# Kernel tuning notes

Hardware: AMD Instinct MI355X
Metric: run time of the kernel (lower is better)

The kernel has to match this reference:

```python
import jax, jax.numpy as jnp
import numpy as np

B, T, E, H = 128, 512, 256, 256  # batch, seqlen, embed_size, latent_size (must be equal E==H)


def gru_cell(x, h, Wih, Whh, bih, bhh):
    # PyTorch GRU gate math. Wih:[3H,E], Whh:[3H,H]
    gi = x @ Wih.T + bih  # [B,3H]
    gh = h @ Whh.T + bhh  # [B,3H]
    i_r, i_z, i_n = jnp.split(gi, 3, axis=-1)
    h_r, h_z, h_n = jnp.split(gh, 3, axis=-1)
    r = jax.nn.sigmoid(i_r + h_r)
    z = jax.nn.sigmoid(i_z + h_z)
    n = jnp.tanh(i_n + r * h_n)
    return (1.0 - z) * n + z * h


def setup_inputs() -> dict:
    key = jax.random.key(0)
    ks = jax.random.split(key, 9)
    s = 1.0 / np.sqrt(H)  # PyTorch default init scale
    return {
        "x": jax.random.normal(ks[0], (B, T, E), dtype=jnp.float32),
        "Wih_e": jax.random.normal(ks[1], (3 * H, E), dtype=jnp.float32) * s,
        "Whh_e": jax.random.normal(ks[2], (3 * H, H), dtype=jnp.float32) * s,
        "bih_e": jax.random.normal(ks[3], (3 * H,), dtype=jnp.float32) * s,
        "bhh_e": jax.random.normal(ks[4], (3 * H,), dtype=jnp.float32) * s,
        "Wih_d": jax.random.normal(ks[5], (3 * H, E), dtype=jnp.float32) * s,
        "Whh_d": jax.random.normal(ks[6], (3 * H, H), dtype=jnp.float32) * s,
        "bih_d": jax.random.normal(ks[7], (3 * H,), dtype=jnp.float32) * s,
        "bhh_d": jax.random.normal(ks[8], (3 * H,), dtype=jnp.float32) * s,
    }


def reference(x, Wih_e, Whh_e, bih_e, bhh_e, Wih_d, Whh_d, bih_d, bhh_d):
    Bs = x.shape[0]
    h0 = jnp.zeros((Bs, H), dtype=x.dtype)

    # ---- encode: nn.GRU, return final hidden state as latents ----
    def enc_step(h, xt):
        return gru_cell(xt, h, Wih_e, Whh_e, bih_e, bhh_e), None

    latents, _ = jax.lax.scan(enc_step, h0, x.transpose(1, 0, 2))  # [B,H]

    # ---- decode: GRUCell unroll; input=prev output, hidden=prev output ----
    def dec_step(carry, _):
        inp, state = carry
        hx = gru_cell(inp, state, Wih_d, Whh_d, bih_d, bhh_d)
        return (hx, hx), hx

    _, ys = jax.lax.scan(dec_step, (latents, h0), None, length=T)  # [T,B,H]
    # original prepends each step's output, so stacked order is reversed
    outputs = jnp.flip(ys, axis=0).transpose(1, 0, 2)  # [B,T,H]
    return outputs, latents
```

## Files before the change

kernel.cpp:

```cpp
#include <hip/hip_runtime.h>


typedef unsigned short u16;
typedef unsigned int   u32;

typedef _Float16 f16x8 __attribute__((ext_vector_type(8)));
typedef float    f32x4 __attribute__((ext_vector_type(4)));

#define B_ 128
#define T_ 512
#define H_ 256
#define G3 768

#define GI_OFF     0ull
#define WIH_OFF    100663296ull
#define WHH_OFF    101056512ull
#define WRZ_OFF    101449728ull
#define WIN_OFF    101711872ull
#define WHN_OFF    101842944ull
#define BG_OFF     101974016ull
#define BHN_E_OFF  101977088ull
#define BDEC_OFF   101978112ull
#define H1_OFF     101982208ull

#define E_WN1_L   0
#define E_STG_L   65536
#define E_HL_L    116736
#define E_BHN_L   133120
#define ENC_LDS   134144

#define D_WHN_L   0
#define D_HL_L    131072
#define D_BIA_L   147456
#define DEC_LDS   151552

__device__ __forceinline__ float h2f(u16 u) {
    return (float)__builtin_bit_cast(_Float16, u);
}
__device__ __forceinline__ u16 f2h(float f) {
    _Float16 h = (_Float16)f;
    return __builtin_bit_cast(u16, h);
}
__device__ __forceinline__ float sigf(float x) {
    return __builtin_amdgcn_rcpf(1.f + __builtin_amdgcn_exp2f(x * -1.4426950408889634f));
}
__device__ __forceinline__ float tanhf_(float x) {
    return 1.f - 2.f * __builtin_amdgcn_rcpf(1.f + __builtin_amdgcn_exp2f(x * 2.8853900817779268f));
}
__device__ __forceinline__ f16x8 ldfrag(const u16* base, int nt, int ks, int l) {
    return __builtin_bit_cast(f16x8, *(const uint4*)(base + ((size_t)((nt * 8 + ks) * 64 + l)) * 8));
}
__device__ __forceinline__ void gload_lds16(const void* g, void* l) {
    __builtin_amdgcn_global_load_lds(
        (const __attribute__((address_space(1))) unsigned int*)(g),
        (__attribute__((address_space(3))) unsigned int*)(l),
        16, 0, 0);
}
#define MFMA16(a, b, c) __builtin_amdgcn_mfma_f32_16x16x32_f16((a), (b), (c), 0, 0, 0)

__global__ __launch_bounds__(256) void prep_kernel(
    const float* __restrict__ Wih_e, const float* __restrict__ Whh_e,
    const float* __restrict__ bih_e, const float* __restrict__ bhh_e,
    const float* __restrict__ Wih_d, const float* __restrict__ Whh_d,
    const float* __restrict__ bih_d, const float* __restrict__ bhh_d,
    char* ws)
{
    int gid = blockIdx.x * 256 + threadIdx.x;
    const int NFRAG = 160 * 8 * 64;
    if (gid < NFRAG) {
        int lane = gid & 63;
        int ks = (gid >> 6) & 7;
        int a = gid >> 9;
        int lm = lane & 15, lg = lane >> 4;
        int k0 = ks * 32 + lg * 8;
        const float* s0; const float* s1 = nullptr; u16* dst; int nt;
        if (a < 48)       { nt = a;       s0 = Wih_e + (size_t)(nt*16+lm)*256 + k0;            dst = (u16*)(ws + WIH_OFF); }
        else if (a < 96)  { nt = a - 48;  s0 = Whh_e + (size_t)(nt*16+lm)*256 + k0;            dst = (u16*)(ws + WHH_OFF); }
        else if (a < 128) { nt = a - 96;  s0 = Wih_d + (size_t)(nt*16+lm)*256 + k0;
                            s1 = Whh_d + (size_t)(nt*16+lm)*256 + k0;                          dst = (u16*)(ws + WRZ_OFF); }
        else if (a < 144) { nt = a - 128; s0 = Wih_d + (size_t)(512+nt*16+lm)*256 + k0;        dst = (u16*)(ws + WIN_OFF); }
        else              { nt = a - 144; s0 = Whh_d + (size_t)(512+nt*16+lm)*256 + k0;        dst = (u16*)(ws + WHN_OFF); }
        u32 wd[4];
        #pragma unroll
        for (int p = 0; p < 4; ++p) {
            float v0 = s0[2*p]   + (s1 ? s1[2*p]   : 0.f);
            float v1 = s0[2*p+1] + (s1 ? s1[2*p+1] : 0.f);
            wd[p] = (u32)f2h(v0) | ((u32)f2h(v1) << 16);
        }
        uint4 o; o.x = wd[0]; o.y = wd[1]; o.z = wd[2]; o.w = wd[3];
        *(uint4*)(dst + ((size_t)((nt * 8 + ks) * 64 + lane)) * 8) = o;
    } else if (gid < NFRAG + 2048) {
        int bid = gid - NFRAG;
        if (bid < 768) {
            ((float*)(ws + BG_OFF))[bid] = bih_e[bid] + (bid < 512 ? bhh_e[bid] : 0.f);
        } else if (bid < 1024) {
            int j = bid - 768;  ((float*)(ws + BHN_E_OFF))[j] = bhh_e[512 + j];
        } else if (bid < 1536) {
            int j = bid - 1024; ((float*)(ws + BDEC_OFF))[j] = bih_d[j] + bhh_d[j];
        } else if (bid < 1792) {
            int j = bid - 1536; ((float*)(ws + BDEC_OFF))[512 + j] = bih_d[512 + j];
        } else {
            int j = bid - 1792; ((float*)(ws + BDEC_OFF))[768 + j] = bhh_d[512 + j];
        }
    }
}

__global__ __launch_bounds__(256) void gemm_gi(const float* __restrict__ x, char* ws)
{
    extern __shared__ char smem[];
    ushort4* xl = (ushort4*)smem;
    const u16* Wfrag = (const u16*)(ws + WIH_OFF);
    const float* bias = (const float*)(ws + BG_OFF);
    u16* gi = (u16*)(ws + GI_OFF);
    int tid = threadIdx.x;
    int m0 = blockIdx.x * 128;
    int n0 = blockIdx.y * 128;
    {
        int row = tid >> 1, half = tid & 1;
        const float* src = x + (size_t)(m0 + row) * 256 + half * 128;
        #pragma unroll
        for (int q = 0; q < 32; ++q) {
            f32x4 v = *(const f32x4*)(src + q * 4);
            int vv = (row << 6) + (half * 32 + q);
            vv ^= ((row & 7) << 1);
            xl[vv] = make_ushort4(f2h(v.x), f2h(v.y), f2h(v.z), f2h(v.w));
        }
    }
    __syncthreads();
    int l = tid & 63, w = tid >> 6;
    int lm = l & 15, lg = l >> 4;
    int gh = w >> 1, mh = w & 1;
    const f32x4 Z4 = {0.f, 0.f, 0.f, 0.f};
    f32x4 acc[4][4];
    #pragma unroll
    for (int a = 0; a < 4; ++a)
        #pragma unroll
        for (int b = 0; b < 4; ++b) acc[a][b] = Z4;
    #pragma unroll
    for (int ks = 0; ks < 8; ++ks) {
        f16x8 xf[4], wf[4];
        #pragma unroll
        for (int mt = 0; mt < 4; ++mt) {
            int row = mh * 64 + mt * 16 + lm;
            int vv = (row << 6) + ((ks * 4 + lg) << 1);
            vv ^= ((row & 7) << 1);
            xf[mt] = __builtin_bit_cast(f16x8, *(const uint4*)&xl[vv]);
        }
        #pragma unroll
        for (int gt = 0; gt < 4; ++gt)
            wf[gt] = ldfrag(Wfrag, (n0 >> 4) + gh * 4 + gt, ks, l);
        #pragma unroll
        for (int gt = 0; gt < 4; ++gt)
            #pragma unroll
            for (int mt = 0; mt < 4; ++mt)
                acc[gt][mt] = MFMA16(wf[gt], xf[mt], acc[gt][mt]);
    }
    #pragma unroll
    for (int gt = 0; gt < 4; ++gt) {
        int g0 = n0 + (gh * 4 + gt) * 16 + lg * 4;
        f32x4 bv = *(const f32x4*)(bias + g0);
        #pragma unroll
        for (int mt = 0; mt < 4; ++mt) {
            int m = m0 + mh * 64 + mt * 16 + lm;
            f32x4 v = acc[gt][mt] + bv;
            *(ushort4*)(gi + (size_t)m * 768 + g0) =
                make_ushort4(f2h(v.x), f2h(v.y), f2h(v.z), f2h(v.w));
        }
    }
}

__global__ __launch_bounds__(512, 2) void enc_kernel(char* ws, float* __restrict__ dout)
{
    extern __shared__ char smem[];
    uint4*   wn1   = (uint4*)(smem + E_WN1_L);
    char*    stg   = smem + E_STG_L;
    ushort4* hl    = (ushort4*)(smem + E_HL_L);
    float*   bhn_l = (float*)(smem + E_BHN_L);
    const u16* Wf = (const u16*)(ws + WHH_OFF);
    const u16* gi = (const u16*)(ws + GI_OFF);
    float* lat = dout + (size_t)B_ * T_ * H_;
    int tid = threadIdx.x;
    int l = tid & 63, w = tid >> 6;
    int lm = l & 15, lg = l >> 4, lg4 = lg * 4;
    int b0 = blockIdx.x * 16;

    if (tid < 256) bhn_l[tid] = ((const float*)(ws + BHN_E_OFF))[tid];
    #pragma unroll
    for (int q = 0; q < 2; ++q) hl[tid + q * 512] = make_ushort4(0, 0, 0, 0);
    #pragma unroll
    for (int p = 0; p < 8; ++p) {
        int u = tid + p * 512;
        int no = u >> 9, ks = (u >> 6) & 7, ll = u & 63;
        wn1[u] = *(const uint4*)(Wf + ((size_t)(((32 + 2 * no + 1) * 8 + ks) * 64 + ll)) * 8);
    }
    f16x8 Wr[2][8], Wz[2][8], Wn0[8];
    #pragma unroll
    for (int i = 0; i < 2; ++i)
        #pragma unroll
        for (int ks = 0; ks < 8; ++ks) {
            Wr[i][ks] = ldfrag(Wf, 2 * w + i, ks, l);
            Wz[i][ks] = ldfrag(Wf, 16 + 2 * w + i, ks, l);
        }
    #pragma unroll
    for (int ks = 0; ks < 8; ++ks) Wn0[ks] = ldfrag(Wf, 32 + 2 * w, ks, l);

    u32 goff[4];
    #pragma unroll
    for (int q = 0; q < 4; ++q) {
        int s = w + q * 8; if (s > 24) s = 24;
        int u = s * 64 + l;
        int row = u / 100, c = u % 100; if (c > 95) c = 95;
        goff[q] = ((u32)(b0 + row) * T_) * G3 + (u32)c * 8;
    }
    {
        #pragma unroll
        for (int q = 0; q < 4; ++q) {
            int s = w + q * 8;
            if (q < 3 || w == 0)
                gload_lds16(gi + goff[q], stg + s * 1024);
        }
    }
    __syncthreads();

    const f32x4 Z4 = {0.f, 0.f, 0.f, 0.f};
    f32x4 hreg[2] = {Z4, Z4};
    int cur = 0;

    for (int t = 0; t < 512; ++t) {
        int nxt = cur ^ 1;
        int tn = (t + 1) & 511;
        {
            char* sb = stg + nxt * 25600;
            #pragma unroll
            for (int q = 0; q < 4; ++q) {
                int s = w + q * 8;
                if (q < 3 || w == 0)
                    gload_lds16(gi + goff[q] + (u32)tn * G3, sb + s * 1024);
            }
        }
        const ushort4* hc = hl + cur * 1024;
        ushort4* hd = hl + nxt * 1024;
        const char* sc = stg + cur * 25600;

        f32x4 aR[2], aZ[2], aN[2];
        #pragma unroll
        for (int i = 0; i < 2; ++i) { aR[i] = Z4; aZ[i] = Z4; aN[i] = Z4; }
        #pragma unroll
        for (int ks = 0; ks < 8; ++ks) {
            int vv = (lm << 6) + ((ks * 4 + lg) << 1);
            vv ^= ((lm & 7) << 1);
            f16x8 hb = __builtin_bit_cast(f16x8, *(const uint4*)&hc[vv]);
            f16x8 wn1v = __builtin_bit_cast(f16x8, wn1[(w * 8 + ks) * 64 + l]);
            aR[0] = MFMA16(Wr[0][ks], hb, aR[0]);
            aZ[0] = MFMA16(Wz[0][ks], hb, aZ[0]);
            aN[0] = MFMA16(Wn0[ks],   hb, aN[0]);
            aR[1] = MFMA16(Wr[1][ks], hb, aR[1]);
            aZ[1] = MFMA16(Wz[1][ks], hb, aZ[1]);
            aN[1] = MFMA16(wn1v,      hb, aN[1]);
        }
        ushort4 hnew[2];
        const char* rb = sc + lm * 1600;
        #pragma unroll
        for (int i = 0; i < 2; ++i) {
            int j0 = (2 * w + i) * 16 + lg4;
            ushort4 gR = *(const ushort4*)(rb + j0 * 2);
            ushort4 gZ = *(const ushort4*)(rb + 512 + j0 * 2);
            ushort4 gN = *(const ushort4*)(rb + 1024 + j0 * 2);
            float bn0 = bhn_l[j0], bn1 = bhn_l[j0 + 1], bn2 = bhn_l[j0 + 2], bn3 = bhn_l[j0 + 3];
            float r0 = sigf(h2f(gR.x) + aR[i].x), z0 = sigf(h2f(gZ.x) + aZ[i].x);
            float n0 = tanhf_(h2f(gN.x) + r0 * (aN[i].x + bn0));
            float h0 = n0 + z0 * (hreg[i].x - n0);
            float r1 = sigf(h2f(gR.y) + aR[i].y), z1 = sigf(h2f(gZ.y) + aZ[i].y);
            float n1 = tanhf_(h2f(gN.y) + r1 * (aN[i].y + bn1));
            float h1 = n1 + z1 * (hreg[i].y - n1);
            float r2 = sigf(h2f(gR.z) + aR[i].z), z2 = sigf(h2f(gZ.z) + aZ[i].z);
            float n2 = tanhf_(h2f(gN.z) + r2 * (aN[i].z + bn2));
            float h2 = n2 + z2 * (hreg[i].z - n2);
            float r3 = sigf(h2f(gR.w) + aR[i].w), z3 = sigf(h2f(gZ.w) + aZ[i].w);
            float n3 = tanhf_(h2f(gN.w) + r3 * (aN[i].w + bn3));
            float h3 = n3 + z3 * (hreg[i].w - n3);
            f32x4 hv = {h0, h1, h2, h3};
            hreg[i] = hv;
            hnew[i] = make_ushort4(f2h(h0), f2h(h1), f2h(h2), f2h(h3));
            if (t == 511) *(f32x4*)(lat + (size_t)(b0 + lm) * 256 + j0) = hv;
        }
        #pragma unroll
        for (int i = 0; i < 2; ++i) {
            int j0 = (2 * w + i) * 16 + lg4;
            int vh = (lm << 6) + (j0 >> 2);
            vh ^= ((lm & 7) << 1);
            hd[vh] = hnew[i];
        }
        __syncthreads();
        cur = nxt;
    }
}

__global__ __launch_bounds__(256) void dec0_kernel(
    const float* __restrict__ Wih_d, const float* __restrict__ bih_d,
    const float* __restrict__ bhh_d, char* ws, float* __restrict__ dout)
{
    __shared__ float latl[256];
    int b = blockIdx.x, j = threadIdx.x;
    const float* latg = dout + (size_t)B_ * T_ * H_;
    latl[j] = latg[(size_t)b * 256 + j];
    __syncthreads();
    const float* wr = Wih_d + (size_t)j * 256;
    const float* wz = Wih_d + (size_t)(256 + j) * 256;
    const float* wn = Wih_d + (size_t)(512 + j) * 256;
    float sr = 0.f, sz = 0.f, sn = 0.f;
    #pragma unroll 4
    for (int k = 0; k < 256; ++k) {
        float h = latl[k];
        sr = fmaf(h, wr[k], sr); sz = fmaf(h, wz[k], sz); sn = fmaf(h, wn[k], sn);
    }
    float r = sigf(sr + bih_d[j] + bhh_d[j]);
    float z = sigf(sz + bih_d[256 + j] + bhh_d[256 + j]);
    float n = tanhf_(sn + bih_d[512 + j] + r * bhh_d[512 + j]);
    float h1v = (1.f - z) * n;
    ((float*)(ws + H1_OFF))[(size_t)b * 256 + j] = h1v;
    dout[((size_t)b * 512 + 511) * 256 + j] = h1v;
}

__global__ __launch_bounds__(512, 2) void dec_kernel(char* ws, float* __restrict__ dout)
{
    extern __shared__ char smem[];
    uint4*   whn    = (uint4*)(smem + D_WHN_L);
    ushort4* hl     = (ushort4*)(smem + D_HL_L);
    float*   bias_l = (float*)(smem + D_BIA_L);
    const u16* Wrzf = (const u16*)(ws + WRZ_OFF);
    const u16* Winf = (const u16*)(ws + WIN_OFF);
    const uint4* Whnf = (const uint4*)(ws + WHN_OFF);
    const float* bdec = (const float*)(ws + BDEC_OFF);
    const float* h1 = (const float*)(ws + H1_OFF);
    int tid = threadIdx.x;
    int l = tid & 63, w = tid >> 6;
    int lm = l & 15, lg = l >> 4, lg4 = lg * 4;
    int b0 = blockIdx.x * 16;

    #pragma unroll
    for (int p = 0; p < 16; ++p) { int u = tid + p * 512; whn[u] = Whnf[u]; }
    #pragma unroll
    for (int q = 0; q < 2; ++q) bias_l[tid + q * 512] = bdec[tid + q * 512];
    #pragma unroll
    for (int q = 0; q < 2; ++q) {
        int u = tid + q * 512;
        int row = u >> 6, cu = u & 63;
        const float* s = h1 + (size_t)(b0 + row) * 256 + cu * 4;
        int vv = u ^ ((row & 7) << 1);
        hl[vv] = make_ushort4(f2h(s[0]), f2h(s[1]), f2h(s[2]), f2h(s[3]));
    }
    f16x8 Wr[2][8], Wz[2][8], Wi[2][8];
    #pragma unroll
    for (int i = 0; i < 2; ++i)
        #pragma unroll
        for (int ks = 0; ks < 8; ++ks) {
            Wr[i][ks] = ldfrag(Wrzf, 2 * w + i, ks, l);
            Wz[i][ks] = ldfrag(Wrzf, 16 + 2 * w + i, ks, l);
            Wi[i][ks] = ldfrag(Winf, 2 * w + i, ks, l);
        }
    const f32x4 Z4 = {0.f, 0.f, 0.f, 0.f};
    f32x4 hreg[2];
    #pragma unroll
    for (int i = 0; i < 2; ++i) {
        int j0 = (2 * w + i) * 16 + lg4;
        hreg[i] = *(const f32x4*)(h1 + (size_t)(b0 + lm) * 256 + j0);
    }
    __syncthreads();
    int cur = 0;

    for (int it = 1; it < 512; ++it) {
        int nxt = cur ^ 1;
        int trow = 511 - it;
        const ushort4* hc = hl + cur * 1024;
        ushort4* hd = hl + nxt * 1024;

        f32x4 aR[2], aZ[2], aI[2], aN[2];
        #pragma unroll
        for (int i = 0; i < 2; ++i) {
            int jb = (2 * w + i) * 16 + lg4;
            aR[i] = *(const f32x4*)(bias_l + jb);
            aZ[i] = *(const f32x4*)(bias_l + 256 + jb);
            aI[i] = *(const f32x4*)(bias_l + 512 + jb);
            aN[i] = Z4;
        }
        #pragma unroll
        for (int ks = 0; ks < 8; ++ks) {
            int vv = (lm << 6) + ((ks * 4 + lg) << 1);
            vv ^= ((lm & 7) << 1);
            f16x8 hb = __builtin_bit_cast(f16x8, *(const uint4*)&hc[vv]);
            f16x8 wn0 = __builtin_bit_cast(f16x8, whn[((2 * w) * 8 + ks) * 64 + l]);
            f16x8 wn1 = __builtin_bit_cast(f16x8, whn[((2 * w + 1) * 8 + ks) * 64 + l]);
            aR[0] = MFMA16(Wr[0][ks], hb, aR[0]);
            aZ[0] = MFMA16(Wz[0][ks], hb, aZ[0]);
            aI[0] = MFMA16(Wi[0][ks], hb, aI[0]);
            aN[0] = MFMA16(wn0,       hb, aN[0]);
            aR[1] = MFMA16(Wr[1][ks], hb, aR[1]);
            aZ[1] = MFMA16(Wz[1][ks], hb, aZ[1]);
            aI[1] = MFMA16(Wi[1][ks], hb, aI[1]);
            aN[1] = MFMA16(wn1,       hb, aN[1]);
        }
        ushort4 hnew[2];
        #pragma unroll
        for (int i = 0; i < 2; ++i) {
            int jb = (2 * w + i) * 16 + lg4;
            float bn0 = bias_l[768 + jb], bn1 = bias_l[768 + jb + 1];
            float bn2 = bias_l[768 + jb + 2], bn3 = bias_l[768 + jb + 3];
            float r0 = sigf(aR[i].x), z0 = sigf(aZ[i].x);
            float n0 = tanhf_(aI[i].x + r0 * (aN[i].x + bn0));
            float h0 = n0 + z0 * (hreg[i].x - n0);
            float r1 = sigf(aR[i].y), z1 = sigf(aZ[i].y);
            float n1 = tanhf_(aI[i].y + r1 * (aN[i].y + bn1));
            float h1v = n1 + z1 * (hreg[i].y - n1);
            float r2 = sigf(aR[i].z), z2 = sigf(aZ[i].z);
            float n2 = tanhf_(aI[i].z + r2 * (aN[i].z + bn2));
            float h2 = n2 + z2 * (hreg[i].z - n2);
            float r3 = sigf(aR[i].w), z3 = sigf(aZ[i].w);
            float n3 = tanhf_(aI[i].w + r3 * (aN[i].w + bn3));
            float h3 = n3 + z3 * (hreg[i].w - n3);
            f32x4 hv = {h0, h1v, h2, h3};
            hreg[i] = hv;
            hnew[i] = make_ushort4(f2h(h0), f2h(h1v), f2h(h2), f2h(h3));
            *(f32x4*)(dout + ((size_t)(b0 + lm) * 512 + trow) * 256 + jb) = hv;
        }
        #pragma unroll
        for (int i = 0; i < 2; ++i) {
            int j0 = (2 * w + i) * 16 + lg4;
            int vh = (lm << 6) + (j0 >> 2);
            vh ^= ((lm & 7) << 1);
            hd[vh] = hnew[i];
        }
        __syncthreads();
        cur = nxt;
    }
}

extern "C" void kernel_launch(void* const* d_in, const int* in_sizes, int n_in,
                              void* d_out, int out_size, void* d_ws, size_t ws_size,
                              hipStream_t stream)
{
    const float* x     = (const float*)d_in[0];
    const float* Wih_e = (const float*)d_in[1];
    const float* Whh_e = (const float*)d_in[2];
    const float* bih_e = (const float*)d_in[3];
    const float* bhh_e = (const float*)d_in[4];
    const float* Wih_d = (const float*)d_in[5];
    const float* Whh_d = (const float*)d_in[6];
    const float* bih_d = (const float*)d_in[7];
    const float* bhh_d = (const float*)d_in[8];
    char* ws = (char*)d_ws;
    float* out = (float*)d_out;

    (void)hipFuncSetAttribute((const void*)gemm_gi, hipFuncAttributeMaxDynamicSharedMemorySize, 65536);
    (void)hipFuncSetAttribute((const void*)enc_kernel, hipFuncAttributeMaxDynamicSharedMemorySize, ENC_LDS);
    (void)hipFuncSetAttribute((const void*)dec_kernel, hipFuncAttributeMaxDynamicSharedMemorySize, DEC_LDS);

    prep_kernel<<<328, 256, 0, stream>>>(Wih_e, Whh_e, bih_e, bhh_e,
                                         Wih_d, Whh_d, bih_d, bhh_d, ws);
    gemm_gi<<<dim3(512, 6), 256, 65536, stream>>>(x, ws);
    enc_kernel<<<8, 512, ENC_LDS, stream>>>(ws, out);
    dec0_kernel<<<128, 256, 0, stream>>>(Wih_d, bih_d, bhh_d, ws, out);
    dec_kernel<<<8, 512, DEC_LDS, stream>>>(ws, out);
}
```

Measured before the change: 2.271 ms.

## Keep all recurrent weight fragments in registers and restructure per-step MFMA chains

```diff
diff --git a/kernel.cpp b/kernel.cpp
--- a/kernel.cpp
+++ b/kernel.cpp
@@ -5,6 +5,7 @@
 typedef unsigned int   u32;
 
 typedef _Float16 f16x8 __attribute__((ext_vector_type(8)));
+typedef _Float16 f16x2 __attribute__((ext_vector_type(2)));
 typedef float    f32x4 __attribute__((ext_vector_type(4)));
 
 #define B_ 128
@@ -23,16 +24,9 @@
 #define BDEC_OFF   101978112ull
 #define H1_OFF     101982208ull
 
-#define E_WN1_L   0
-#define E_STG_L   65536
-#define E_HL_L    116736
-#define E_BHN_L   133120
-#define ENC_LDS   134144
-
-#define D_WHN_L   0
-#define D_HL_L    131072
-#define D_BIA_L   147456
-#define DEC_LDS   151552
+#define E_STG_L   0
+#define E_HL_L    51200
+#define ENC_LDS   67584
 
 __device__ __forceinline__ float h2f(u16 u) {
     return (float)__builtin_bit_cast(_Float16, u);
@@ -40,6 +34,9 @@
 __device__ __forceinline__ u16 f2h(float f) {
     _Float16 h = (_Float16)f;
     return __builtin_bit_cast(u16, h);
+}
+__device__ __forceinline__ u32 pk2(float a, float b) {
+    return __builtin_bit_cast(u32, __builtin_amdgcn_cvt_pkrtz(a, b));
 }
 __device__ __forceinline__ float sigf(float x) {
     return __builtin_amdgcn_rcpf(1.f + __builtin_amdgcn_exp2f(x * -1.4426950408889634f));
@@ -172,10 +169,8 @@
 __global__ __launch_bounds__(512, 2) void enc_kernel(char* ws, float* __restrict__ dout)
 {
     extern __shared__ char smem[];
-    uint4*   wn1   = (uint4*)(smem + E_WN1_L);
-    char*    stg   = smem + E_STG_L;
-    ushort4* hl    = (ushort4*)(smem + E_HL_L);
-    float*   bhn_l = (float*)(smem + E_BHN_L);
+    char*    stg = smem + E_STG_L;
+    ushort4* hl  = (ushort4*)(smem + E_HL_L);
     const u16* Wf = (const u16*)(ws + WHH_OFF);
     const u16* gi = (const u16*)(ws + GI_OFF);
     float* lat = dout + (size_t)B_ * T_ * H_;
@@ -184,25 +179,22 @@
     int lm = l & 15, lg = l >> 4, lg4 = lg * 4;
     int b0 = blockIdx.x * 16;
 
-    if (tid < 256) bhn_l[tid] = ((const float*)(ws + BHN_E_OFF))[tid];
     #pragma unroll
     for (int q = 0; q < 2; ++q) hl[tid + q * 512] = make_ushort4(0, 0, 0, 0);
-    #pragma unroll
-    for (int p = 0; p < 8; ++p) {
-        int u = tid + p * 512;
-        int no = u >> 9, ks = (u >> 6) & 7, ll = u & 63;
-        wn1[u] = *(const uint4*)(Wf + ((size_t)(((32 + 2 * no + 1) * 8 + ks) * 64 + ll)) * 8);
-    }
-    f16x8 Wr[2][8], Wz[2][8], Wn0[8];
+
+    f16x8 Wr[2][8], Wz[2][8], Wn[2][8];
     #pragma unroll
     for (int i = 0; i < 2; ++i)
         #pragma unroll
         for (int ks = 0; ks < 8; ++ks) {
             Wr[i][ks] = ldfrag(Wf, 2 * w + i, ks, l);
             Wz[i][ks] = ldfrag(Wf, 16 + 2 * w + i, ks, l);
-        }
-    #pragma unroll
-    for (int ks = 0; ks < 8; ++ks) Wn0[ks] = ldfrag(Wf, 32 + 2 * w, ks, l);
+            Wn[i][ks] = ldfrag(Wf, 32 + 2 * w + i, ks, l);
+        }
+    f32x4 bnb[2];
+    #pragma unroll
+    for (int i = 0; i < 2; ++i)
+        bnb[i] = *(const f32x4*)((const float*)(ws + BHN_E_OFF) + (2 * w + i) * 16 + lg4);
 
     u32 goff[4];
     #pragma unroll
@@ -240,56 +232,55 @@
         }
         const ushort4* hc = hl + cur * 1024;
         ushort4* hd = hl + nxt * 1024;
-        const char* sc = stg + cur * 25600;
-
-        f32x4 aR[2], aZ[2], aN[2];
-        #pragma unroll
-        for (int i = 0; i < 2; ++i) { aR[i] = Z4; aZ[i] = Z4; aN[i] = Z4; }
+        const char* rb = stg + cur * 25600 + lm * 1600;
+
+        f16x8 hb[8];
         #pragma unroll
         for (int ks = 0; ks < 8; ++ks) {
             int vv = (lm << 6) + ((ks * 4 + lg) << 1);
             vv ^= ((lm & 7) << 1);
-            f16x8 hb = __builtin_bit_cast(f16x8, *(const uint4*)&hc[vv]);
-            f16x8 wn1v = __builtin_bit_cast(f16x8, wn1[(w * 8 + ks) * 64 + l]);
-            aR[0] = MFMA16(Wr[0][ks], hb, aR[0]);
-            aZ[0] = MFMA16(Wz[0][ks], hb, aZ[0]);
-            aN[0] = MFMA16(Wn0[ks],   hb, aN[0]);
-            aR[1] = MFMA16(Wr[1][ks], hb, aR[1]);
-            aZ[1] = MFMA16(Wz[1][ks], hb, aZ[1]);
-            aN[1] = MFMA16(wn1v,      hb, aN[1]);
-        }
-        ushort4 hnew[2];
-        const char* rb = sc + lm * 1600;
+            hb[ks] = __builtin_bit_cast(f16x8, *(const uint4*)&hc[vv]);
+        }
+        ushort4 gR[2], gZ[2], gN[2];
         #pragma unroll
         for (int i = 0; i < 2; ++i) {
             int j0 = (2 * w + i) * 16 + lg4;
-            ushort4 gR = *(const ushort4*)(rb + j0 * 2);
-            ushort4 gZ = *(const ushort4*)(rb + 512 + j0 * 2);
-            ushort4 gN = *(const ushort4*)(rb + 1024 + j0 * 2);
-            float bn0 = bhn_l[j0], bn1 = bhn_l[j0 + 1], bn2 = bhn_l[j0 + 2], bn3 = bhn_l[j0 + 3];
-            float r0 = sigf(h2f(gR.x) + aR[i].x), z0 = sigf(h2f(gZ.x) + aZ[i].x);
-            float n0 = tanhf_(h2f(gN.x) + r0 * (aN[i].x + bn0));
+            gR[i] = *(const ushort4*)(rb + j0 * 2);
+            gZ[i] = *(const ushort4*)(rb + 512 + j0 * 2);
+            gN[i] = *(const ushort4*)(rb + 1024 + j0 * 2);
+        }
+        #pragma unroll
+        for (int i = 0; i < 2; ++i) {
+            int j0 = (2 * w + i) * 16 + lg4;
+            f32x4 aR = {h2f(gR[i].x), h2f(gR[i].y), h2f(gR[i].z), h2f(gR[i].w)};
+            f32x4 aZ = {h2f(gZ[i].x), h2f(gZ[i].y), h2f(gZ[i].z), h2f(gZ[i].w)};
+            f32x4 aN = Z4;
+            __builtin_amdgcn_s_setprio(1);
+            #pragma unroll
+            for (int ks = 0; ks < 8; ++ks) {
+                aR = MFMA16(Wr[i][ks], hb[ks], aR);
+                aZ = MFMA16(Wz[i][ks], hb[ks], aZ);
+                aN = MFMA16(Wn[i][ks], hb[ks], aN);
+            }
+            __builtin_amdgcn_s_setprio(0);
+            float r0 = sigf(aR.x), z0 = sigf(aZ.x);
+            float n0 = tanhf_(h2f(gN[i].x) + r0 * (aN.x + bnb[i].x));
             float h0 = n0 + z0 * (hreg[i].x - n0);
-            float r1 = sigf(h2f(gR.y) + aR[i].y), z1 = sigf(h2f(gZ.y) + aZ[i].y);
-            float n1 = tanhf_(h2f(gN.y) + r1 * (aN[i].y + bn1));
+            float r1 = sigf(aR.y), z1 = sigf(aZ.y);
+            float n1 = tanhf_(h2f(gN[i].y) + r1 * (aN.y + bnb[i].y));
             float h1 = n1 + z1 * (hreg[i].y - n1);
-            float r2 = sigf(h2f(gR.z) + aR[i].z), z2 = sigf(h2f(gZ.z) + aZ[i].z);
-            float n2 = tanhf_(h2f(gN.z) + r2 * (aN[i].z + bn2));
+            float r2 = sigf(aR.z), z2 = sigf(aZ.z);
+            float n2 = tanhf_(h2f(gN[i].z) + r2 * (aN.z + bnb[i].z));
             float h2 = n2 + z2 * (hreg[i].z - n2);
-            float r3 = sigf(h2f(gR.w) + aR[i].w), z3 = sigf(h2f(gZ.w) + aZ[i].w);
-            float n3 = tanhf_(h2f(gN.w) + r3 * (aN[i].w + bn3));
+            float r3 = sigf(aR.w), z3 = sigf(aZ.w);
+            float n3 = tanhf_(h2f(gN[i].w) + r3 * (aN.w + bnb[i].w));
             float h3 = n3 + z3 * (hreg[i].w - n3);
             f32x4 hv = {h0, h1, h2, h3};
             hreg[i] = hv;
-            hnew[i] = make_ushort4(f2h(h0), f2h(h1), f2h(h2), f2h(h3));
-            if (t == 511) *(f32x4*)(lat + (size_t)(b0 + lm) * 256 + j0) = hv;
-        }
-        #pragma unroll
-        for (int i = 0; i < 2; ++i) {
-            int j0 = (2 * w + i) * 16 + lg4;
             int vh = (lm << 6) + (j0 >> 2);
             vh ^= ((lm & 7) << 1);
-            hd[vh] = hnew[i];
+            *(uint2*)&hd[vh] = make_uint2(pk2(h0, h1), pk2(h2, h3));
+            if (t == 511) *(f32x4*)(lat + (size_t)(b0 + lm) * 256 + j0) = hv;
         }
         __syncthreads();
         cur = nxt;
@@ -324,13 +315,10 @@
 
 __global__ __launch_bounds__(512, 2) void dec_kernel(char* ws, float* __restrict__ dout)
 {
-    extern __shared__ char smem[];
-    uint4*   whn    = (uint4*)(smem + D_WHN_L);
-    ushort4* hl     = (ushort4*)(smem + D_HL_L);
-    float*   bias_l = (float*)(smem + D_BIA_L);
+    __shared__ ushort4 hl[2][1024];
     const u16* Wrzf = (const u16*)(ws + WRZ_OFF);
     const u16* Winf = (const u16*)(ws + WIN_OFF);
-    const uint4* Whnf = (const uint4*)(ws + WHN_OFF);
+    const u16* Whnf = (const u16*)(ws + WHN_OFF);
     const float* bdec = (const float*)(ws + BDEC_OFF);
     const float* h1 = (const float*)(ws + H1_OFF);
     int tid = threadIdx.x;
@@ -339,18 +327,14 @@
     int b0 = blockIdx.x * 16;
 
     #pragma unroll
-    for (int p = 0; p < 16; ++p) { int u = tid + p * 512; whn[u] = Whnf[u]; }
-    #pragma unroll
-    for (int q = 0; q < 2; ++q) bias_l[tid + q * 512] = bdec[tid + q * 512];
-    #pragma unroll
     for (int q = 0; q < 2; ++q) {
         int u = tid + q * 512;
         int row = u >> 6, cu = u & 63;
         const float* s = h1 + (size_t)(b0 + row) * 256 + cu * 4;
         int vv = u ^ ((row & 7) << 1);
-        hl[vv] = make_ushort4(f2h(s[0]), f2h(s[1]), f2h(s[2]), f2h(s[3]));
-    }
-    f16x8 Wr[2][8], Wz[2][8], Wi[2][8];
+        hl[0][vv] = make_ushort4(f2h(s[0]), f2h(s[1]), f2h(s[2]), f2h(s[3]));
+    }
+    f16x8 Wr[2][8], Wz[2][8], Wi[2][8], Wn[2][8];
     #pragma unroll
     for (int i = 0; i < 2; ++i)
         #pragma unroll
@@ -358,7 +342,17 @@
             Wr[i][ks] = ldfrag(Wrzf, 2 * w + i, ks, l);
             Wz[i][ks] = ldfrag(Wrzf, 16 + 2 * w + i, ks, l);
             Wi[i][ks] = ldfrag(Winf, 2 * w + i, ks, l);
-        }
+            Wn[i][ks] = ldfrag(Whnf, 2 * w + i, ks, l);
+        }
+    f32x4 bR[2], bZ[2], bI[2], bN[2];
+    #pragma unroll
+    for (int i = 0; i < 2; ++i) {
+        int jb = (2 * w + i) * 16 + lg4;
+        bR[i] = *(const f32x4*)(bdec + jb);
+        bZ[i] = *(const f32x4*)(bdec + 256 + jb);
+        bI[i] = *(const f32x4*)(bdec + 512 + jb);
+        bN[i] = *(const f32x4*)(bdec + 768 + jb);
+    }
     const f32x4 Z4 = {0.f, 0.f, 0.f, 0.f};
     f32x4 hreg[2];
     #pragma unroll
@@ -372,63 +366,47 @@
     for (int it = 1; it < 512; ++it) {
         int nxt = cur ^ 1;
         int trow = 511 - it;
-        const ushort4* hc = hl + cur * 1024;
-        ushort4* hd = hl + nxt * 1024;
-
-        f32x4 aR[2], aZ[2], aI[2], aN[2];
-        #pragma unroll
-        for (int i = 0; i < 2; ++i) {
-            int jb = (2 * w + i) * 16 + lg4;
-            aR[i] = *(const f32x4*)(bias_l + jb);
-            aZ[i] = *(const f32x4*)(bias_l + 256 + jb);
-            aI[i] = *(const f32x4*)(bias_l + 512 + jb);
-            aN[i] = Z4;
-        }
+        const ushort4* hc = hl[cur];
+        ushort4* hd = hl[nxt];
+
+        f16x8 hb[8];
         #pragma unroll
         for (int ks = 0; ks < 8; ++ks) {
             int vv = (lm << 6) + ((ks * 4 + lg) << 1);
             vv ^= ((lm & 7) << 1);
-            f16x8 hb = __builtin_bit_cast(f16x8, *(const uint4*)&hc[vv]);
-            f16x8 wn0 = __builtin_bit_cast(f16x8, whn[((2 * w) * 8 + ks) * 64 + l]);
-            f16x8 wn1 = __builtin_bit_cast(f16x8, whn[((2 * w + 1) * 8 + ks) * 64 + l]);
-            aR[0] = MFMA16(Wr[0][ks], hb, aR[0]);
-            aZ[0] = MFMA16(Wz[0][ks], hb, aZ[0]);
-            aI[0] = MFMA16(Wi[0][ks], hb, aI[0]);
-            aN[0] = MFMA16(wn0,       hb, aN[0]);
-            aR[1] = MFMA16(Wr[1][ks], hb, aR[1]);
-            aZ[1] = MFMA16(Wz[1][ks], hb, aZ[1]);
-            aI[1] = MFMA16(Wi[1][ks], hb, aI[1]);
-            aN[1] = MFMA16(wn1,       hb, aN[1]);
-        }
-        ushort4 hnew[2];
+            hb[ks] = __builtin_bit_cast(f16x8, *(const uint4*)&hc[vv]);
+        }
         #pragma unroll
         for (int i = 0; i < 2; ++i) {
             int jb = (2 * w + i) * 16 + lg4;
-            float bn0 = bias_l[768 + jb], bn1 = bias_l[768 + jb + 1];
-            float bn2 = bias_l[768 + jb + 2], bn3 = bias_l[768 + jb + 3];
-            float r0 = sigf(aR[i].x), z0 = sigf(aZ[i].x);
-            float n0 = tanhf_(aI[i].x + r0 * (aN[i].x + bn0));
+            f32x4 aR = bR[i], aZ = bZ[i], aI = bI[i], aN = Z4;
+            __builtin_amdgcn_s_setprio(1);
+            #pragma unroll
+            for (int ks = 0; ks < 8; ++ks) {
+                aR = MFMA16(Wr[i][ks], hb[ks], aR);
+                aZ = MFMA16(Wz[i][ks], hb[ks], aZ);
+                aI = MFMA16(Wi[i][ks], hb[ks], aI);
+                aN = MFMA16(Wn[i][ks], hb[ks], aN);
+            }
+            __builtin_amdgcn_s_setprio(0);
+            float r0 = sigf(aR.x), z0 = sigf(aZ.x);
+            float n0 = tanhf_(aI.x + r0 * (aN.x + bN[i].x));
             float h0 = n0 + z0 * (hreg[i].x - n0);
-            float r1 = sigf(aR[i].y), z1 = sigf(aZ[i].y);
-            float n1 = tanhf_(aI[i].y + r1 * (aN[i].y + bn1));
+            float r1 = sigf(aR.y), z1 = sigf(aZ.y);
+            float n1 = tanhf_(aI.y + r1 * (aN.y + bN[i].y));
             float h1v = n1 + z1 * (hreg[i].y - n1);
-            float r2 = sigf(aR[i].z), z2 = sigf(aZ[i].z);
-            float n2 = tanhf_(aI[i].z + r2 * (aN[i].z + bn2));
+            float r2 = sigf(aR.z), z2 = sigf(aZ.z);
+            float n2 = tanhf_(aI.z + r2 * (aN.z + bN[i].z));
             float h2 = n2 + z2 * (hreg[i].z - n2);
-            float r3 = sigf(aR[i].w), z3 = sigf(aZ[i].w);
-            float n3 = tanhf_(aI[i].w + r3 * (aN[i].w + bn3));
+            float r3 = sigf(aR.w), z3 = sigf(aZ.w);
+            float n3 = tanhf_(aI.w + r3 * (aN.w + bN[i].w));
             float h3 = n3 + z3 * (hreg[i].w - n3);
             f32x4 hv = {h0, h1v, h2, h3};
             hreg[i] = hv;
-            hnew[i] = make_ushort4(f2h(h0), f2h(h1v), f2h(h2), f2h(h3));
+            int vh = (lm << 6) + (jb >> 2);
+            vh ^= ((lm & 7) << 1);
+            *(uint2*)&hd[vh] = make_uint2(pk2(h0, h1v), pk2(h2, h3));
             *(f32x4*)(dout + ((size_t)(b0 + lm) * 512 + trow) * 256 + jb) = hv;
-        }
-        #pragma unroll
-        for (int i = 0; i < 2; ++i) {
-            int j0 = (2 * w + i) * 16 + lg4;
-            int vh = (lm << 6) + (j0 >> 2);
-            vh ^= ((lm & 7) << 1);
-            hd[vh] = hnew[i];
         }
         __syncthreads();
         cur = nxt;
@@ -453,12 +431,11 @@
 
     (void)hipFuncSetAttribute((const void*)gemm_gi, hipFuncAttributeMaxDynamicSharedMemorySize, 65536);
     (void)hipFuncSetAttribute((const void*)enc_kernel, hipFuncAttributeMaxDynamicSharedMemorySize, ENC_LDS);
-    (void)hipFuncSetAttribute((const void*)dec_kernel, hipFuncAttributeMaxDynamicSharedMemorySize, DEC_LDS);
 
     prep_kernel<<<328, 256, 0, stream>>>(Wih_e, Whh_e, bih_e, bhh_e,
                                          Wih_d, Whh_d, bih_d, bhh_d, ws);
     gemm_gi<<<dim3(512, 6), 256, 65536, stream>>>(x, ws);
     enc_kernel<<<8, 512, ENC_LDS, stream>>>(ws, out);
     dec0_kernel<<<128, 256, 0, stream>>>(Wih_d, bih_d, bhh_d, ws, out);
-    dec_kernel<<<8, 512, DEC_LDS, stream>>>(ws, out);
-}
+    dec_kernel<<<8, 512, 0, stream>>>(ws, out);
+}
```

Result: slower. 5.240 ms (+130.7%).
